# Kernel optimization log

Measured on AMD Instinct MI355X. Metric: run time of the kernel, lower is better.

## Reference

```python
import jax, jax.numpy as jnp
import numpy as np

E = 4096          # num edges
M = 12            # sum(m_size) = 5+4+3
C = 64            # sphere_channels
D = 64            # m_output_channels
M0 = 5            # m_size[0]
XD = 64           # extra_m0_output_channels
EC = 128          # edge channel dims (edge_channels_list = [128,128,128])
MAIN = M * C * D          # 49152
EXTRA = M0 * C * XD       # 20480
TOTAL = MAIN + EXTRA      # 69632


def setup_inputs() -> dict:
    key = jax.random.key(0)
    ks = jax.random.split(key, 8)
    def xavier(k, shape):
        fan_in, fan_out = shape
        lim = jnp.sqrt(6.0 / (fan_in + fan_out))
        return jax.random.uniform(k, shape, jnp.float32, -lim, lim)
    return {
        "x": jax.random.normal(ks[0], (E, M, C), jnp.float32),
        "x_edge": jax.random.normal(ks[1], (E, EC), jnp.float32),
        "W1": xavier(ks[2], (EC, EC)),
        "b1": jnp.zeros((EC,), jnp.float32),
        "W2": xavier(ks[3], (EC, EC)),
        "b2": jnp.zeros((EC,), jnp.float32),
        "W3": xavier(ks[4], (EC, TOTAL)),
        "b3": jnp.zeros((TOTAL,), jnp.float32),
    }


def reference(x, x_edge, W1, b1, W2, b2, W3, b3):
    # edge MLP: Dense -> silu -> Dense -> silu -> Dense
    h = jax.nn.silu(x_edge @ W1 + b1)
    h = jax.nn.silu(h @ W2 + b2)
    edge_weights = h @ W3 + b3                      # (E, TOTAL) huge intermediate
    main_w = edge_weights[:, :MAIN].reshape(E, M, C, D)
    out = jnp.einsum('bmcd,bmc->bmd', main_w, x)    # (E, M, D)
    extra_w = edge_weights[:, MAIN:].reshape(E, M0, C, XD)
    x_0 = x[:, :M0, :]
    x_0_gating = jnp.einsum('bmcd,bmc->bd', extra_w, x_0)  # (E, XD)
    return out, x_0_gating
```

## Files before the change

kernel.cpp:

```cpp
#include <hip/hip_runtime.h>
#include <hip/hip_bf16.h>

#define E 4096
#define M 12
#define C 64
#define D 64
#define M0 5
#define XD 64
#define EC 128
#define MAIN (M*C*D)
#define EXTRA (M0*C*XD)
#define TOTAL (MAIN+EXTRA)
#define NSLICE 17
#define KDIM 8256
#define NKB 43

typedef float  f32x4  __attribute__((ext_vector_type(4)));
typedef __bf16 bf16x8 __attribute__((ext_vector_type(8)));
typedef unsigned int u32x4 __attribute__((ext_vector_type(4)));
typedef unsigned int u32x2 __attribute__((ext_vector_type(2)));

typedef const __attribute__((address_space(1))) void gvoid;
typedef __attribute__((address_space(3))) void lvoid;

__device__ __forceinline__ float silu_f(float v) { return v / (1.0f + __expf(-v)); }

__device__ __forceinline__ unsigned short f2bf(float f) {
    unsigned u = __builtin_bit_cast(unsigned, f);
    u += 0x7FFFu + ((u >> 16) & 1u);
    return (unsigned short)(u >> 16);
}
__device__ __forceinline__ unsigned pack2(float a, float b) {
    return (unsigned)f2bf(a) | ((unsigned)f2bf(b) << 16);
}
__device__ __forceinline__ float asf(unsigned u) { return __builtin_bit_cast(float, u); }

__global__ __launch_bounds__(256) void mlp_kernel(
    const float* __restrict__ x_edge, const float* __restrict__ W1,
    const float* __restrict__ b1, const float* __restrict__ W2,
    const float* __restrict__ b2, unsigned short* __restrict__ h2t)
{
    __shared__ float xe[16][128];
    __shared__ float h1s[16][128];
    const int t  = threadIdx.x;
    const int b0 = blockIdx.x * 16;
    const int j  = t & 127;
    const int rh = t >> 7;

    #pragma unroll
    for (int i = 0; i < 8; ++i) {
        int lin = t + i * 256;
        int r = lin >> 7, k = lin & 127;
        xe[r][k] = x_edge[(size_t)(b0 + r) * EC + k];
    }
    __syncthreads();
    {
        float acc[8];
        float bb = b1[j];
        #pragma unroll
        for (int it = 0; it < 8; ++it) acc[it] = bb;
        for (int k = 0; k < 128; ++k) {
            float w = W1[k * EC + j];
            #pragma unroll
            for (int it = 0; it < 8; ++it) acc[it] += xe[rh + it * 2][k] * w;
        }
        #pragma unroll
        for (int it = 0; it < 8; ++it) h1s[rh + it * 2][j] = silu_f(acc[it]);
    }
    __syncthreads();
    {
        float acc[8];
        float bb = b2[j];
        #pragma unroll
        for (int it = 0; it < 8; ++it) acc[it] = bb;
        for (int k = 0; k < 128; ++k) {
            float w = W2[k * EC + j];
            #pragma unroll
            for (int it = 0; it < 8; ++it) acc[it] += h1s[rh + it * 2][k] * w;
        }
        #pragma unroll
        for (int it = 0; it < 8; ++it)
            h2t[(size_t)j * E + (b0 + rh + it * 2)] = f2bf(silu_f(acc[it]));
    }
    if (t < 16) h2t[(size_t)128 * E + b0 + t] = 0x3F80;
}

__global__ __launch_bounds__(256) void w3t_kernel(
    const float* __restrict__ W3, const float* __restrict__ b3,
    unsigned short* __restrict__ w3t)
{
    const int k = blockIdx.x;
    const int s = blockIdx.y;
    __shared__ float tile[64][68];
    const int t = threadIdx.x;
    const float* src = ((k < 128) ? (W3 + (size_t)k * TOTAL) : b3) + s * 4096;

    const int c  = t >> 2;
    const int dp = (t & 3) * 16;
    #pragma unroll
    for (int i = 0; i < 4; ++i) {
        float4 v = *reinterpret_cast<const float4*>(src + c * 64 + dp + i * 4);
        *reinterpret_cast<float4*>(&tile[c][dp + i * 4]) = v;
    }
    __syncthreads();

    const int d  = t >> 2;
    const int cp = (t & 3) * 16;
    unsigned u[8];
    #pragma unroll
    for (int i = 0; i < 8; ++i)
        u[i] = pack2(tile[cp + 2 * i][d], tile[cp + 2 * i + 1][d]);
    unsigned short* dst = w3t + (size_t)(s * 64 + d) * KDIM + k * 64 + cp;
    *reinterpret_cast<u32x4*>(dst)     = u32x4{u[0], u[1], u[2], u[3]};
    *reinterpret_cast<u32x4*>(dst + 8) = u32x4{u[4], u[5], u[6], u[7]};
}

__global__ __launch_bounds__(256, 3) void gemm_kernel(
    const float* __restrict__ x, const unsigned short* __restrict__ h2t,
    const unsigned short* __restrict__ w3t, float* __restrict__ out,
    unsigned short* __restrict__ outp, unsigned short* __restrict__ gatep)
{
    __shared__ __align__(16) unsigned short h2s[NKB * 256];
    __shared__ __align__(16) unsigned short Bs[3][4096];

    const int t  = threadIdx.x;
    const int w  = t >> 6;
    const int l  = t & 63;
    const int p  = l >> 4;
    const int lr = l & 15;

    const int bid  = blockIdx.x;
    const int slot = (bid & 7) * 102 + (bid >> 3);
    const int grp  = slot >> 4;
    const int bx   = slot & 15;
    const int s    = grp / 3;
    const int kz   = grp % 3;
    const int k0   = kz * NKB;
    const int b0   = bx * 256;
    const int m    = (s < 12) ? s : (s - 12);

    {
        const char* h2g = (const char*)(h2t + (size_t)k0 * E + b0);
        for (int lin = t * 16; lin < NKB * 512; lin += 4096) {
            int kl = lin >> 9, off = lin & 511;
            *reinterpret_cast<u32x4*>((char*)h2s + lin) =
                *reinterpret_cast<const u32x4*>(h2g + (size_t)kl * (E * 2) + off);
        }
    }

    u32x4 xa[4][2];
    #pragma unroll
    for (int rf = 0; rf < 4; ++rf)
        #pragma unroll
        for (int s2 = 0; s2 < 2; ++s2) {
            const float* xp = x + (size_t)(b0 + w * 64 + rf * 16 + lr) * (M * C)
                              + m * 64 + s2 * 32 + p * 8;
            float4 a = *reinterpret_cast<const float4*>(xp);
            float4 b = *reinterpret_cast<const float4*>(xp + 4);
            xa[rf][s2] = u32x4{pack2(a.x, a.y), pack2(a.z, a.w),
                               pack2(b.x, b.y), pack2(b.z, b.w)};
        }

    const unsigned short* gsrc[2];
    #pragma unroll
    for (int q = 0; q < 2; ++q)
        gsrc[q] = w3t + (size_t)(s * 64 + w * 16 + lr) * KDIM
                  + (size_t)k0 * 64 + (q * 4 + p) * 8;

#define STAGE(buf, kr)                                                          \
    {                                                                           \
        _Pragma("unroll")                                                       \
        for (int q = 0; q < 2; ++q)                                             \
            __builtin_amdgcn_global_load_lds(                                   \
                (gvoid*)(gsrc[q] + (size_t)(kr) * 64),                          \
                (lvoid*)(&Bs[buf][(w * 2 + q) * 512]), 16, 0, 0);               \
    }

    f32x4 acc[4][4];
    #pragma unroll
    for (int a = 0; a < 4; ++a)
        #pragma unroll
        for (int b = 0; b < 4; ++b) acc[a][b] = f32x4{0.f, 0.f, 0.f, 0.f};
    const f32x4 zf = {0.f, 0.f, 0.f, 0.f};

#define KBODY(kr, curv)                                                         \
    {                                                                           \
        float h[4][4];                                                          \
        _Pragma("unroll")                                                       \
        for (int rf = 0; rf < 4; ++rf) {                                        \
            u32x2 hv = *reinterpret_cast<const u32x2*>(                         \
                &h2s[(kr) * 256 + w * 64 + rf * 16 + p * 4]);                   \
            h[rf][0] = asf(hv.x << 16);                                         \
            h[rf][1] = asf(hv.x & 0xFFFF0000u);                                 \
            h[rf][2] = asf(hv.y << 16);                                         \
            h[rf][3] = asf(hv.y & 0xFFFF0000u);                                 \
        }                                                                       \
        __builtin_amdgcn_s_setprio(1);                                          \
        _Pragma("unroll")                                                       \
        for (int cf = 0; cf < 4; ++cf) {                                        \
            u32x4 B0 = *reinterpret_cast<const u32x4*>(                         \
                &Bs[curv][(cf * 2 + 0) * 512 + l * 8]);                         \
            u32x4 B1 = *reinterpret_cast<const u32x4*>(                         \
                &Bs[curv][(cf * 2 + 1) * 512 + l * 8]);                         \
            _Pragma("unroll")                                                   \
            for (int rf = 0; rf < 4; ++rf) {                                    \
                f32x4 tt = __builtin_amdgcn_mfma_f32_16x16x32_bf16(             \
                    __builtin_bit_cast(bf16x8, xa[rf][0]),                      \
                    __builtin_bit_cast(bf16x8, B0), zf, 0, 0, 0);               \
                tt = __builtin_amdgcn_mfma_f32_16x16x32_bf16(                   \
                    __builtin_bit_cast(bf16x8, xa[rf][1]),                      \
                    __builtin_bit_cast(bf16x8, B1), tt, 0, 0, 0);               \
                acc[rf][cf][0] += h[rf][0] * tt[0];                             \
                acc[rf][cf][1] += h[rf][1] * tt[1];                             \
                acc[rf][cf][2] += h[rf][2] * tt[2];                             \
                acc[rf][cf][3] += h[rf][3] * tt[3];                             \
            }                                                                   \
        }                                                                       \
        __builtin_amdgcn_s_setprio(0);                                          \
    }

    __syncthreads();

    STAGE(0, 0);
    STAGE(1, 1);

    int cur = 0;
    #pragma unroll 1
    for (int kr = 0; kr < NKB - 2; ++kr) {
        asm volatile("s_waitcnt vmcnt(2) lgkmcnt(0)" ::: "memory");
        __builtin_amdgcn_s_barrier();
        int nxt = (cur == 0) ? 2 : cur - 1;
        STAGE(nxt, kr + 2);
        KBODY(kr, cur);
        cur = (cur == 2) ? 0 : cur + 1;
    }
    asm volatile("s_waitcnt vmcnt(2) lgkmcnt(0)" ::: "memory");
    __builtin_amdgcn_s_barrier();
    KBODY(NKB - 2, cur);
    cur = (cur == 2) ? 0 : cur + 1;
    asm volatile("s_waitcnt vmcnt(0) lgkmcnt(0)" ::: "memory");
    __builtin_amdgcn_s_barrier();
    KBODY(NKB - 1, cur);
#undef STAGE
#undef KBODY

    if (s < 12) {
        if (kz == 0) {
            #pragma unroll
            for (int rf = 0; rf < 4; ++rf)
                #pragma unroll
                for (int cf = 0; cf < 4; ++cf)
                    #pragma unroll
                    for (int r = 0; r < 4; ++r) {
                        int b = b0 + w * 64 + rf * 16 + p * 4 + r;
                        int d = cf * 16 + lr;
                        out[(size_t)b * (M * D) + s * D + d] = acc[rf][cf][r];
                    }
        } else {
            unsigned short* ob = outp + (size_t)(kz - 1) * (E * M * D);
            #pragma unroll
            for (int rf = 0; rf < 4; ++rf)
                #pragma unroll
                for (int cf = 0; cf < 4; ++cf)
                    #pragma unroll
                    for (int r = 0; r < 4; ++r) {
                        int b = b0 + w * 64 + rf * 16 + p * 4 + r;
                        int d = cf * 16 + lr;
                        ob[(size_t)b * (M * D) + s * D + d] = f2bf(acc[rf][cf][r]);
                    }
        }
    } else {
        unsigned short* gp = gatep + (size_t)((s - 12) * 3 + kz) * (E * 64);
        #pragma unroll
        for (int rf = 0; rf < 4; ++rf)
            #pragma unroll
            for (int cf = 0; cf < 4; ++cf)
                #pragma unroll
                for (int r = 0; r < 4; ++r) {
                    int b = b0 + w * 64 + rf * 16 + p * 4 + r;
                    int d = cf * 16 + lr;
                    gp[(size_t)b * 64 + d] = f2bf(acc[rf][cf][r]);
                }
    }
}

__global__ __launch_bounds__(256) void reduce_kernel(
    float* __restrict__ out, const unsigned short* __restrict__ outp,
    const unsigned short* __restrict__ gatep)
{
    const int MAIN4 = E * M * D / 4;
    int i = blockIdx.x * 256 + threadIdx.x;
    if (i < MAIN4) {
        float4 a = reinterpret_cast<float4*>(out)[i];
        u32x2 p0 = *reinterpret_cast<const u32x2*>(outp + (size_t)i * 4);
        u32x2 p1 = *reinterpret_cast<const u32x2*>(outp + (size_t)E * M * D + (size_t)i * 4);
        a.x += asf(p0.x << 16)         + asf(p1.x << 16);
        a.y += asf(p0.x & 0xFFFF0000u) + asf(p1.x & 0xFFFF0000u);
        a.z += asf(p0.y << 16)         + asf(p1.y << 16);
        a.w += asf(p0.y & 0xFFFF0000u) + asf(p1.y & 0xFFFF0000u);
        reinterpret_cast<float4*>(out)[i] = a;
    } else {
        int j = i - MAIN4;
        float4 sum = make_float4(0.f, 0.f, 0.f, 0.f);
        #pragma unroll
        for (int q = 0; q < 15; ++q) {
            u32x2 v = *reinterpret_cast<const u32x2*>(
                gatep + (size_t)q * (E * 64) + (size_t)j * 4);
            sum.x += asf(v.x << 16);
            sum.y += asf(v.x & 0xFFFF0000u);
            sum.z += asf(v.y << 16);
            sum.w += asf(v.y & 0xFFFF0000u);
        }
        reinterpret_cast<float4*>(out + (size_t)E * M * D)[j] = sum;
    }
}

extern "C" void kernel_launch(void* const* d_in, const int* in_sizes, int n_in,
                              void* d_out, int out_size, void* d_ws, size_t ws_size,
                              hipStream_t stream)
{
    const float* x      = (const float*)d_in[0];
    const float* x_edge = (const float*)d_in[1];
    const float* W1     = (const float*)d_in[2];
    const float* b1     = (const float*)d_in[3];
    const float* W2     = (const float*)d_in[4];
    const float* b2     = (const float*)d_in[5];
    const float* W3     = (const float*)d_in[6];
    const float* b3     = (const float*)d_in[7];

    float* out = (float*)d_out;

    char* ws = (char*)d_ws;
    unsigned short* w3t   = (unsigned short*)ws;
    unsigned short* h2t   = (unsigned short*)(ws + 17965056);
    unsigned short* outp  = (unsigned short*)(ws + 19021824);
    unsigned short* gatep = (unsigned short*)(ws + 31604736);

    mlp_kernel<<<E / 16, 256, 0, stream>>>(x_edge, W1, b1, W2, b2, h2t);
    w3t_kernel<<<dim3(129, NSLICE), 256, 0, stream>>>(W3, b3, w3t);
    gemm_kernel<<<816, 256, 0, stream>>>(x, h2t, w3t, out, outp, gatep);
    reduce_kernel<<<3328, 256, 0, stream>>>(out, outp, gatep);
}
```

Baseline: 149.7 us.

## Replace LDS-staged GEMM pipeline with register double-buffered global loads and split D

```diff
diff --git a/kernel.cpp b/kernel.cpp
--- a/kernel.cpp
+++ b/kernel.cpp
@@ -20,9 +20,6 @@
 typedef unsigned int u32x4 __attribute__((ext_vector_type(4)));
 typedef unsigned int u32x2 __attribute__((ext_vector_type(2)));
 
-typedef const __attribute__((address_space(1))) void gvoid;
-typedef __attribute__((address_space(3))) void lvoid;
-
 __device__ __forceinline__ float silu_f(float v) { return v / (1.0f + __expf(-v)); }
 
 __device__ __forceinline__ unsigned short f2bf(float f) {
@@ -120,9 +117,6 @@
     const unsigned short* __restrict__ w3t, float* __restrict__ out,
     unsigned short* __restrict__ outp, unsigned short* __restrict__ gatep)
 {
-    __shared__ __align__(16) unsigned short h2s[NKB * 256];
-    __shared__ __align__(16) unsigned short Bs[3][4096];
-
     const int t  = threadIdx.x;
     const int w  = t >> 6;
     const int l  = t & 63;
@@ -130,23 +124,16 @@
     const int lr = l & 15;
 
     const int bid  = blockIdx.x;
-    const int slot = (bid & 7) * 102 + (bid >> 3);
+    const int slot = (bid & 7) * 204 + (bid >> 3);
     const int grp  = slot >> 4;
     const int bx   = slot & 15;
-    const int s    = grp / 3;
-    const int kz   = grp % 3;
+    const int dh   = grp & 1;
+    const int g2   = grp >> 1;
+    const int s    = g2 / 3;
+    const int kz   = g2 % 3;
     const int k0   = kz * NKB;
     const int b0   = bx * 256;
     const int m    = (s < 12) ? s : (s - 12);
-
-    {
-        const char* h2g = (const char*)(h2t + (size_t)k0 * E + b0);
-        for (int lin = t * 16; lin < NKB * 512; lin += 4096) {
-            int kl = lin >> 9, off = lin & 511;
-            *reinterpret_cast<u32x4*>((char*)h2s + lin) =
-                *reinterpret_cast<const u32x4*>(h2g + (size_t)kl * (E * 2) + off);
-        }
-    }
 
     u32x4 xa[4][2];
     #pragma unroll
@@ -161,55 +148,53 @@
                                pack2(b.x, b.y), pack2(b.z, b.w)};
         }
 
-    const unsigned short* gsrc[2];
-    #pragma unroll
-    for (int q = 0; q < 2; ++q)
-        gsrc[q] = w3t + (size_t)(s * 64 + w * 16 + lr) * KDIM
-                  + (size_t)k0 * 64 + (q * 4 + p) * 8;
-
-#define STAGE(buf, kr)                                                          \
+    const unsigned short* bp0 = w3t + (size_t)(s * 64 + dh * 32 + lr) * KDIM
+                                + (size_t)k0 * 64 + p * 8;
+    const unsigned short* bp1 = bp0 + (size_t)16 * KDIM;
+    const unsigned short* hp = h2t + (size_t)k0 * E + b0 + w * 64 + p * 4;
+
+    f32x4 acc[4][2];
+    #pragma unroll
+    for (int a = 0; a < 4; ++a)
+        #pragma unroll
+        for (int b = 0; b < 2; ++b) acc[a][b] = f32x4{0.f, 0.f, 0.f, 0.f};
+    const f32x4 zf = {0.f, 0.f, 0.f, 0.f};
+
+    u32x4 BA[2][2], BB[2][2];
+    u32x2 hA[4], hB[4];
+
+#define ISSUE(BUF, HUF, KB, KH)                                                 \
     {                                                                           \
+        BUF[0][0] = *reinterpret_cast<const u32x4*>(bp0 + (KB));                \
+        BUF[0][1] = *reinterpret_cast<const u32x4*>(bp0 + (KB) + 32);           \
+        BUF[1][0] = *reinterpret_cast<const u32x4*>(bp1 + (KB));                \
+        BUF[1][1] = *reinterpret_cast<const u32x4*>(bp1 + (KB) + 32);           \
         _Pragma("unroll")                                                       \
-        for (int q = 0; q < 2; ++q)                                             \
-            __builtin_amdgcn_global_load_lds(                                   \
-                (gvoid*)(gsrc[q] + (size_t)(kr) * 64),                          \
-                (lvoid*)(&Bs[buf][(w * 2 + q) * 512]), 16, 0, 0);               \
-    }
-
-    f32x4 acc[4][4];
-    #pragma unroll
-    for (int a = 0; a < 4; ++a)
-        #pragma unroll
-        for (int b = 0; b < 4; ++b) acc[a][b] = f32x4{0.f, 0.f, 0.f, 0.f};
-    const f32x4 zf = {0.f, 0.f, 0.f, 0.f};
-
-#define KBODY(kr, curv)                                                         \
+        for (int rf = 0; rf < 4; ++rf)                                          \
+            HUF[rf] = *reinterpret_cast<const u32x2*>(hp + (KH) + rf * 16);     \
+    }
+
+#define COMPUTE(BUF, HUF)                                                       \
     {                                                                           \
         float h[4][4];                                                          \
         _Pragma("unroll")                                                       \
         for (int rf = 0; rf < 4; ++rf) {                                        \
-            u32x2 hv = *reinterpret_cast<const u32x2*>(                         \
-                &h2s[(kr) * 256 + w * 64 + rf * 16 + p * 4]);                   \
-            h[rf][0] = asf(hv.x << 16);                                         \
-            h[rf][1] = asf(hv.x & 0xFFFF0000u);                                 \
-            h[rf][2] = asf(hv.y << 16);                                         \
-            h[rf][3] = asf(hv.y & 0xFFFF0000u);                                 \
+            h[rf][0] = asf(HUF[rf].x << 16);                                    \
+            h[rf][1] = asf(HUF[rf].x & 0xFFFF0000u);                            \
+            h[rf][2] = asf(HUF[rf].y << 16);                                    \
+            h[rf][3] = asf(HUF[rf].y & 0xFFFF0000u);                            \
         }                                                                       \
         __builtin_amdgcn_s_setprio(1);                                          \
         _Pragma("unroll")                                                       \
-        for (int cf = 0; cf < 4; ++cf) {                                        \
-            u32x4 B0 = *reinterpret_cast<const u32x4*>(                         \
-                &Bs[curv][(cf * 2 + 0) * 512 + l * 8]);                         \
-            u32x4 B1 = *reinterpret_cast<const u32x4*>(                         \
-                &Bs[curv][(cf * 2 + 1) * 512 + l * 8]);                         \
+        for (int cf = 0; cf < 2; ++cf) {                                        \
             _Pragma("unroll")                                                   \
             for (int rf = 0; rf < 4; ++rf) {                                    \
                 f32x4 tt = __builtin_amdgcn_mfma_f32_16x16x32_bf16(             \
                     __builtin_bit_cast(bf16x8, xa[rf][0]),                      \
-                    __builtin_bit_cast(bf16x8, B0), zf, 0, 0, 0);               \
+                    __builtin_bit_cast(bf16x8, BUF[cf][0]), zf, 0, 0, 0);       \
                 tt = __builtin_amdgcn_mfma_f32_16x16x32_bf16(                   \
                     __builtin_bit_cast(bf16x8, xa[rf][1]),                      \
-                    __builtin_bit_cast(bf16x8, B1), tt, 0, 0, 0);               \
+                    __builtin_bit_cast(bf16x8, BUF[cf][1]), tt, 0, 0, 0);       \
                 acc[rf][cf][0] += h[rf][0] * tt[0];                             \
                 acc[rf][cf][1] += h[rf][1] * tt[1];                             \
                 acc[rf][cf][2] += h[rf][2] * tt[2];                             \
@@ -219,41 +204,40 @@
         __builtin_amdgcn_s_setprio(0);                                          \
     }
 
-    __syncthreads();
-
-    STAGE(0, 0);
-    STAGE(1, 1);
-
-    int cur = 0;
+    ISSUE(BA, hA, 0, 0);
+    ISSUE(BB, hB, 64, E);
+    bp0 += 128; bp1 += 128; hp += 2 * E;
+
     #pragma unroll 1
-    for (int kr = 0; kr < NKB - 2; ++kr) {
-        asm volatile("s_waitcnt vmcnt(2) lgkmcnt(0)" ::: "memory");
-        __builtin_amdgcn_s_barrier();
-        int nxt = (cur == 0) ? 2 : cur - 1;
-        STAGE(nxt, kr + 2);
-        KBODY(kr, cur);
-        cur = (cur == 2) ? 0 : cur + 1;
-    }
-    asm volatile("s_waitcnt vmcnt(2) lgkmcnt(0)" ::: "memory");
-    __builtin_amdgcn_s_barrier();
-    KBODY(NKB - 2, cur);
-    cur = (cur == 2) ? 0 : cur + 1;
-    asm volatile("s_waitcnt vmcnt(0) lgkmcnt(0)" ::: "memory");
-    __builtin_amdgcn_s_barrier();
-    KBODY(NKB - 1, cur);
-#undef STAGE
-#undef KBODY
+    for (int i = 0; i < 20; ++i) {
+        asm volatile("s_waitcnt vmcnt(8)" ::: "memory");
+        COMPUTE(BA, hA);
+        ISSUE(BA, hA, 0, 0);
+        asm volatile("s_waitcnt vmcnt(8)" ::: "memory");
+        COMPUTE(BB, hB);
+        ISSUE(BB, hB, 64, E);
+        bp0 += 128; bp1 += 128; hp += 2 * E;
+    }
+    asm volatile("s_waitcnt vmcnt(8)" ::: "memory");
+    COMPUTE(BA, hA);
+    ISSUE(BA, hA, 0, 0);
+    asm volatile("s_waitcnt vmcnt(8)" ::: "memory");
+    COMPUTE(BB, hB);
+    asm volatile("s_waitcnt vmcnt(0)" ::: "memory");
+    COMPUTE(BA, hA);
+#undef ISSUE
+#undef COMPUTE
 
     if (s < 12) {
         if (kz == 0) {
             #pragma unroll
             for (int rf = 0; rf < 4; ++rf)
                 #pragma unroll
-                for (int cf = 0; cf < 4; ++cf)
+                for (int cf = 0; cf < 2; ++cf)
                     #pragma unroll
                     for (int r = 0; r < 4; ++r) {
                         int b = b0 + w * 64 + rf * 16 + p * 4 + r;
-                        int d = cf * 16 + lr;
+                        int d = dh * 32 + cf * 16 + lr;
                         out[(size_t)b * (M * D) + s * D + d] = acc[rf][cf][r];
                     }
         } else {
@@ -261,11 +245,11 @@
             #pragma unroll
             for (int rf = 0; rf < 4; ++rf)
                 #pragma unroll
-                for (int cf = 0; cf < 4; ++cf)
+                for (int cf = 0; cf < 2; ++cf)
                     #pragma unroll
                     for (int r = 0; r < 4; ++r) {
                         int b = b0 + w * 64 + rf * 16 + p * 4 + r;
-                        int d = cf * 16 + lr;
+                        int d = dh * 32 + cf * 16 + lr;
                         ob[(size_t)b * (M * D) + s * D + d] = f2bf(acc[rf][cf][r]);
                     }
         }
@@ -274,11 +258,11 @@
         #pragma unroll
         for (int rf = 0; rf < 4; ++rf)
             #pragma unroll
-            for (int cf = 0; cf < 4; ++cf)
+            for (int cf = 0; cf < 2; ++cf)
                 #pragma unroll
                 for (int r = 0; r < 4; ++r) {
                     int b = b0 + w * 64 + rf * 16 + p * 4 + r;
-                    int d = cf * 16 + lr;
+                    int d = dh * 32 + cf * 16 + lr;
                     gp[(size_t)b * 64 + d] = f2bf(acc[rf][cf][r]);
                 }
     }
@@ -338,6 +322,6 @@
 
     mlp_kernel<<<E / 16, 256, 0, stream>>>(x_edge, W1, b1, W2, b2, h2t);
     w3t_kernel<<<dim3(129, NSLICE), 256, 0, stream>>>(W3, b3, w3t);
-    gemm_kernel<<<816, 256, 0, stream>>>(x, h2t, w3t, out, outp, gatep);
+    gemm_kernel<<<1632, 256, 0, stream>>>(x, h2t, w3t, out, outp, gatep);
     reduce_kernel<<<3328, 256, 0, stream>>>(out, outp, gatep);
 }
```

Result: slower. 359.2 us (+139.9%).

## Stream h2 tiles through pipelined LDS stages and process two k-blocks per barrier

Applied to the files above, without the earlier changes.

```diff
diff --git a/kernel.cpp b/kernel.cpp
--- a/kernel.cpp
+++ b/kernel.cpp
@@ -120,8 +120,8 @@
     const unsigned short* __restrict__ w3t, float* __restrict__ out,
     unsigned short* __restrict__ outp, unsigned short* __restrict__ gatep)
 {
-    __shared__ __align__(16) unsigned short h2s[NKB * 256];
-    __shared__ __align__(16) unsigned short Bs[3][4096];
+    __shared__ __align__(16) unsigned short BsB[3][2][4096];
+    __shared__ __align__(16) unsigned short Bsh[3][2][256];
 
     const int t  = threadIdx.x;
     const int w  = t >> 6;
@@ -139,15 +139,6 @@
     const int b0   = bx * 256;
     const int m    = (s < 12) ? s : (s - 12);
 
-    {
-        const char* h2g = (const char*)(h2t + (size_t)k0 * E + b0);
-        for (int lin = t * 16; lin < NKB * 512; lin += 4096) {
-            int kl = lin >> 9, off = lin & 511;
-            *reinterpret_cast<u32x4*>((char*)h2s + lin) =
-                *reinterpret_cast<const u32x4*>(h2g + (size_t)kl * (E * 2) + off);
-        }
-    }
-
     u32x4 xa[4][2];
     #pragma unroll
     for (int rf = 0; rf < 4; ++rf)
@@ -161,19 +152,41 @@
                                pack2(b.x, b.y), pack2(b.z, b.w)};
         }
 
+    u32x2 h42[4];
+    #pragma unroll
+    for (int rf = 0; rf < 4; ++rf)
+        h42[rf] = *reinterpret_cast<const u32x2*>(
+            h2t + (size_t)(k0 + 42) * E + b0 + w * 64 + rf * 16 + p * 4);
+
     const unsigned short* gsrc[2];
     #pragma unroll
     for (int q = 0; q < 2; ++q)
         gsrc[q] = w3t + (size_t)(s * 64 + w * 16 + lr) * KDIM
                   + (size_t)k0 * 64 + (q * 4 + p) * 8;
 
-#define STAGE(buf, kr)                                                          \
+    const unsigned short* hsrc = h2t + (size_t)(k0 + (w >> 1)) * E + b0
+                                 + (w & 1) * 128 + l * 2;
+
+#define STAGE2(buf, pr)                                                         \
+    {                                                                           \
+        _Pragma("unroll")                                                       \
+        for (int rr = 0; rr < 2; ++rr)                                          \
+            _Pragma("unroll")                                                   \
+            for (int q = 0; q < 2; ++q)                                         \
+                __builtin_amdgcn_global_load_lds(                               \
+                    (gvoid*)(gsrc[q] + (size_t)(2 * (pr) + rr) * 64),           \
+                    (lvoid*)(&BsB[buf][rr][(w * 2 + q) * 512]), 16, 0, 0);      \
+        __builtin_amdgcn_global_load_lds(                                       \
+            (gvoid*)(hsrc + (size_t)(2 * (pr)) * E),                            \
+            (lvoid*)((char*)&Bsh[buf][0][0] + w * 256), 4, 0, 0);               \
+    }
+#define STAGE1(buf)                                                             \
     {                                                                           \
         _Pragma("unroll")                                                       \
         for (int q = 0; q < 2; ++q)                                             \
             __builtin_amdgcn_global_load_lds(                                   \
-                (gvoid*)(gsrc[q] + (size_t)(kr) * 64),                          \
-                (lvoid*)(&Bs[buf][(w * 2 + q) * 512]), 16, 0, 0);               \
+                (gvoid*)(gsrc[q] + (size_t)42 * 64),                            \
+                (lvoid*)(&BsB[buf][0][(w * 2 + q) * 512]), 16, 0, 0);           \
     }
 
     f32x4 acc[4][4];
@@ -183,13 +196,13 @@
         for (int b = 0; b < 4; ++b) acc[a][b] = f32x4{0.f, 0.f, 0.f, 0.f};
     const f32x4 zf = {0.f, 0.f, 0.f, 0.f};
 
-#define KBODY(kr, curv)                                                         \
+#define KBODY(curv, rr)                                                         \
     {                                                                           \
         float h[4][4];                                                          \
         _Pragma("unroll")                                                       \
         for (int rf = 0; rf < 4; ++rf) {                                        \
             u32x2 hv = *reinterpret_cast<const u32x2*>(                         \
-                &h2s[(kr) * 256 + w * 64 + rf * 16 + p * 4]);                   \
+                &Bsh[curv][rr][w * 64 + rf * 16 + p * 4]);                      \
             h[rf][0] = asf(hv.x << 16);                                         \
             h[rf][1] = asf(hv.x & 0xFFFF0000u);                                 \
             h[rf][2] = asf(hv.y << 16);                                         \
@@ -199,9 +212,9 @@
         _Pragma("unroll")                                                       \
         for (int cf = 0; cf < 4; ++cf) {                                        \
             u32x4 B0 = *reinterpret_cast<const u32x4*>(                         \
-                &Bs[curv][(cf * 2 + 0) * 512 + l * 8]);                         \
+                &BsB[curv][rr][(cf * 2 + 0) * 512 + l * 8]);                    \
             u32x4 B1 = *reinterpret_cast<const u32x4*>(                         \
-                &Bs[curv][(cf * 2 + 1) * 512 + l * 8]);                         \
+                &BsB[curv][rr][(cf * 2 + 1) * 512 + l * 8]);                    \
             _Pragma("unroll")                                                   \
             for (int rf = 0; rf < 4; ++rf) {                                    \
                 f32x4 tt = __builtin_amdgcn_mfma_f32_16x16x32_bf16(             \
@@ -218,31 +231,70 @@
         }                                                                       \
         __builtin_amdgcn_s_setprio(0);                                          \
     }
-
-    __syncthreads();
-
-    STAGE(0, 0);
-    STAGE(1, 1);
+#define KBODY42()                                                               \
+    {                                                                           \
+        float h[4][4];                                                          \
+        _Pragma("unroll")                                                       \
+        for (int rf = 0; rf < 4; ++rf) {                                        \
+            h[rf][0] = asf(h42[rf].x << 16);                                    \
+            h[rf][1] = asf(h42[rf].x & 0xFFFF0000u);                            \
+            h[rf][2] = asf(h42[rf].y << 16);                                    \
+            h[rf][3] = asf(h42[rf].y & 0xFFFF0000u);                            \
+        }                                                                       \
+        __builtin_amdgcn_s_setprio(1);                                          \
+        _Pragma("unroll")                                                       \
+        for (int cf = 0; cf < 4; ++cf) {                                        \
+            u32x4 B0 = *reinterpret_cast<const u32x4*>(                         \
+                &BsB[0][0][(cf * 2 + 0) * 512 + l * 8]);                        \
+            u32x4 B1 = *reinterpret_cast<const u32x4*>(                         \
+                &BsB[0][0][(cf * 2 + 1) * 512 + l * 8]);                        \
+            _Pragma("unroll")                                                   \
+            for (int rf = 0; rf < 4; ++rf) {                                    \
+                f32x4 tt = __builtin_amdgcn_mfma_f32_16x16x32_bf16(             \
+                    __builtin_bit_cast(bf16x8, xa[rf][0]),                      \
+                    __builtin_bit_cast(bf16x8, B0), zf, 0, 0, 0);               \
+                tt = __builtin_amdgcn_mfma_f32_16x16x32_bf16(                   \
+                    __builtin_bit_cast(bf16x8, xa[rf][1]),                      \
+                    __builtin_bit_cast(bf16x8, B1), tt, 0, 0, 0);               \
+                acc[rf][cf][0] += h[rf][0] * tt[0];                             \
+                acc[rf][cf][1] += h[rf][1] * tt[1];                             \
+                acc[rf][cf][2] += h[rf][2] * tt[2];                             \
+                acc[rf][cf][3] += h[rf][3] * tt[3];                             \
+            }                                                                   \
+        }                                                                       \
+        __builtin_amdgcn_s_setprio(0);                                          \
+    }
+
+    STAGE2(0, 0);
+    STAGE2(1, 1);
 
     int cur = 0;
     #pragma unroll 1
-    for (int kr = 0; kr < NKB - 2; ++kr) {
-        asm volatile("s_waitcnt vmcnt(2) lgkmcnt(0)" ::: "memory");
+    for (int pr = 0; pr < 19; ++pr) {
+        asm volatile("s_waitcnt vmcnt(5) lgkmcnt(0)" ::: "memory");
         __builtin_amdgcn_s_barrier();
         int nxt = (cur == 0) ? 2 : cur - 1;
-        STAGE(nxt, kr + 2);
-        KBODY(kr, cur);
+        STAGE2(nxt, pr + 2);
+        KBODY(cur, 0);
+        KBODY(cur, 1);
         cur = (cur == 2) ? 0 : cur + 1;
     }
+    asm volatile("s_waitcnt vmcnt(5) lgkmcnt(0)" ::: "memory");
+    __builtin_amdgcn_s_barrier();
+    STAGE1(0);
+    KBODY(1, 0);
+    KBODY(1, 1);
     asm volatile("s_waitcnt vmcnt(2) lgkmcnt(0)" ::: "memory");
     __builtin_amdgcn_s_barrier();
-    KBODY(NKB - 2, cur);
-    cur = (cur == 2) ? 0 : cur + 1;
+    KBODY(2, 0);
+    KBODY(2, 1);
     asm volatile("s_waitcnt vmcnt(0) lgkmcnt(0)" ::: "memory");
     __builtin_amdgcn_s_barrier();
-    KBODY(NKB - 1, cur);
-#undef STAGE
+    KBODY42();
+#undef STAGE2
+#undef STAGE1
 #undef KBODY
+#undef KBODY42
 
     if (s < 12) {
         if (kz == 0) {
```

Result: slower. 575.6 us (+284.4%).
